# Kernel tuning notes

Measured on AMD Instinct MI355X. Metric: run time of the kernel, lower is better.

## Reference

```python
import jax, jax.numpy as jnp
import numpy as np

N_NODES = 50000
F_IN = 96
HIDDEN = 128
OUT = 64
N_EDGES = 800000


def setup_inputs() -> dict:
    key = jax.random.key(0)
    ks = jax.random.split(key, 8)
    x = jax.random.normal(ks[0], (N_NODES, F_IN), dtype=jnp.float32)
    edge_index = jax.random.randint(ks[1], (2, N_EDGES), 0, N_NODES, dtype=jnp.int64)
    s = 1.0 / np.sqrt(F_IN)
    W1_rel = jax.random.uniform(ks[2], (HIDDEN, F_IN), minval=-s, maxval=s, dtype=jnp.float32)
    b1 = jax.random.uniform(ks[3], (HIDDEN,), minval=-s, maxval=s, dtype=jnp.float32)
    W1_root = jax.random.uniform(ks[4], (HIDDEN, F_IN), minval=-s, maxval=s, dtype=jnp.float32)
    s2 = 1.0 / np.sqrt(HIDDEN)
    W2_rel = jax.random.uniform(ks[5], (OUT, HIDDEN), minval=-s2, maxval=s2, dtype=jnp.float32)
    b2 = jax.random.uniform(ks[6], (OUT,), minval=-s2, maxval=s2, dtype=jnp.float32)
    W2_root = jax.random.uniform(ks[7], (OUT, HIDDEN), minval=-s2, maxval=s2, dtype=jnp.float32)
    return {"x": x, "edge_index": edge_index, "W1_rel": W1_rel, "b1": b1,
            "W1_root": W1_root, "W2_rel": W2_rel, "b2": b2, "W2_root": W2_root}


def _graph_conv(x, src, dst, mask, W_rel, b, W_root):
    # messages = x[src] (masked to remove self-loops), sum-aggregated at dst
    msgs = x[src] * mask  # [E, F]
    agg = jax.ops.segment_sum(msgs, dst, num_segments=x.shape[0])  # [N, F]
    return agg @ W_rel.T + b + x @ W_root.T


def reference(x, edge_index, W1_rel, b1, W1_root, W2_rel, b2, W2_root):
    src, dst = edge_index[0], edge_index[1]
    # remove_self_loops: zero out contributions of edges with src == dst
    mask = (src != dst).astype(x.dtype)[:, None]  # [E, 1]
    h = jax.nn.relu(_graph_conv(x, src, dst, mask, W1_rel, b1, W1_root))
    out = _graph_conv(h, src, dst, mask, W2_rel, b2, W2_root)
    return out
```

## Files before the change

kernel.cpp:

```cpp
#include <hip/hip_runtime.h>


#define N_NODES 50000
#define F_IN    96
#define HIDDEN  128
#define OUT_F   64
#define DCAP    64

typedef __attribute__((ext_vector_type(8))) short short8;
typedef __attribute__((ext_vector_type(4))) float floatx4;

__device__ inline unsigned short f2bf(float f) {
    union { float f; unsigned u; } v; v.f = f;
    unsigned r = v.u + 0x7FFF + ((v.u >> 16) & 1);
    return (unsigned short)(r >> 16);
}
__device__ inline float bf2f(unsigned short b) {
    union { unsigned u; float f; } v; v.u = ((unsigned)b) << 16;
    return v.f;
}

__global__ __launch_bounds__(256) void setup_kernel(
    const float* __restrict__ x,
    const float* __restrict__ W1_rel, const float* __restrict__ W1_root,
    const float* __restrict__ W2_rel, const float* __restrict__ W2_root,
    unsigned short* __restrict__ xb, unsigned short* __restrict__ W1b,
    unsigned short* __restrict__ W2rb, unsigned short* __restrict__ W2sb,
    int* __restrict__ degz, int total8, int nzero)
{
    int i = blockIdx.x * 256 + threadIdx.x;
    if (i < total8) {
        const float4* p = (const float4*)(x + (size_t)i * 8);
        float4 v0 = p[0], v1 = p[1];
        short8 o;
        o[0] = (short)f2bf(v0.x); o[1] = (short)f2bf(v0.y);
        o[2] = (short)f2bf(v0.z); o[3] = (short)f2bf(v0.w);
        o[4] = (short)f2bf(v1.x); o[5] = (short)f2bf(v1.y);
        o[6] = (short)f2bf(v1.z); o[7] = (short)f2bf(v1.w);
        *(short8*)(xb + (size_t)i * 8) = o;
    }
    if (i < nzero) degz[i] = 0;
    if (i < 128 * 192) {
        int j = i / 192, k = i % 192;
        float v = (k < 96) ? W1_rel[j * 96 + k] : W1_root[j * 96 + k - 96];
        W1b[i] = f2bf(v);
    } else if (i < 128 * 192 + 64 * 128) {
        int i2 = i - 128 * 192;
        W2rb[i2] = f2bf(W2_rel[i2]);
    } else if (i < 128 * 192 + 2 * 64 * 128) {
        int i3 = i - 128 * 192 - 64 * 128;
        W2sb[i3] = f2bf(W2_root[i3]);
    }
}

__global__ __launch_bounds__(256) void place_kernel(
    const int* __restrict__ ei, int* __restrict__ deg,
    int* __restrict__ csr, int E, int slice_size)
{
    int sl = blockIdx.x & 7;
    int i4 = (blockIdx.x >> 3) * 256 + threadIdx.x;
    int E4 = E >> 2;
    if (i4 < E4) {
        int4 d4 = ((const int4*)(ei + E))[i4];
        int e0 = i4 * 4;
        int dd[4] = {d4.x, d4.y, d4.z, d4.w};
        #pragma unroll
        for (int k = 0; k < 4; ++k) {
            int d = dd[k];
            if ((unsigned)d >= (unsigned)N_NODES) continue;
            if (d / slice_size != sl) continue;
            int s = ei[e0 + k];
            if (s == d) continue;
            int r = atomicAdd(&deg[d], 1);
            if (r < DCAP) csr[d * DCAP + r] = s;
        }
    } else if (i4 == E4) {
        for (int e = E4 * 4; e < E; ++e) {
            int d = ei[E + e];
            if ((unsigned)d >= (unsigned)N_NODES) continue;
            if (d / slice_size != sl) continue;
            int s = ei[e];
            if (s == d) continue;
            int r = atomicAdd(&deg[d], 1);
            if (r < DCAP) csr[d * DCAP + r] = s;
        }
    }
}

template<int F>
__device__ inline void gather_row8(const unsigned short* __restrict__ feat,
                                   const int* __restrict__ csr, int j, int end,
                                   float* acc)
{
    const unsigned short* fc = feat;
    for (; j + 3 < end; j += 4) {
        int s0 = csr[j], s1 = csr[j + 1], s2 = csr[j + 2], s3 = csr[j + 3];
        s0 = ((unsigned)s0 < (unsigned)N_NODES) ? s0 : 0;
        s1 = ((unsigned)s1 < (unsigned)N_NODES) ? s1 : 0;
        s2 = ((unsigned)s2 < (unsigned)N_NODES) ? s2 : 0;
        s3 = ((unsigned)s3 < (unsigned)N_NODES) ? s3 : 0;
        short8 v0 = *(const short8*)(fc + (size_t)s0 * F);
        short8 v1 = *(const short8*)(fc + (size_t)s1 * F);
        short8 v2 = *(const short8*)(fc + (size_t)s2 * F);
        short8 v3 = *(const short8*)(fc + (size_t)s3 * F);
        #pragma unroll
        for (int i = 0; i < 8; ++i)
            acc[i] += (bf2f((unsigned short)v0[i]) + bf2f((unsigned short)v1[i]))
                    + (bf2f((unsigned short)v2[i]) + bf2f((unsigned short)v3[i]));
    }
    for (; j < end; ++j) {
        int s0 = csr[j];
        s0 = ((unsigned)s0 < (unsigned)N_NODES) ? s0 : 0;
        short8 v0 = *(const short8*)(fc + (size_t)s0 * F);
        #pragma unroll
        for (int i = 0; i < 8; ++i) acc[i] += bf2f((unsigned short)v0[i]);
    }
}

__global__ __launch_bounds__(256) void gemm1_fused(
    const unsigned short* __restrict__ xb, const unsigned short* __restrict__ W1b,
    const float* __restrict__ b1, const int* __restrict__ deg,
    const int* __restrict__ csr, unsigned short* __restrict__ h, int N)
{
    __shared__ __align__(16) unsigned short aggs[32][104];
    const int tid = threadIdx.x;
    const int node0 = blockIdx.x * 32;

    for (int task = tid; task < 384; task += 256) {
        int nl = task / 12, c = task % 12;
        int node = node0 + nl;
        float acc[8] = {};
        if (node < N) {
            int dg = deg[node];
            if (dg > DCAP) dg = DCAP;
            int j = node * DCAP;
            gather_row8<F_IN>(xb + c * 8, csr, j, j + dg, acc);
        }
        short8 o;
        #pragma unroll
        for (int i = 0; i < 8; ++i) o[i] = (short)f2bf(acc[i]);
        *(short8*)&aggs[nl][c * 8] = o;
    }
    __syncthreads();

    const int lane = tid & 63;
    const int wave = tid >> 6;
    const int m = lane & 15, quad = lane >> 4;
    const int node_base = node0 + (wave & 1) * 16;
    const int jt0 = (wave >> 1) * 4;
    int na = node_base + m;
    if (na >= N) na = N - 1;
    short8 a[6];
    #pragma unroll
    for (int c = 0; c < 3; ++c)
        a[c] = *(const short8*)&aggs[(wave & 1) * 16 + m][c * 32 + quad * 8];
    #pragma unroll
    for (int c = 0; c < 3; ++c)
        a[3 + c] = *(const short8*)(xb + (size_t)na * 96 + c * 32 + quad * 8);
    #pragma unroll
    for (int jt = 0; jt < 4; ++jt) {
        floatx4 acc = {0.f, 0.f, 0.f, 0.f};
        const unsigned short* wb = W1b + (size_t)((jt0 + jt) * 16 + m) * 192 + quad * 8;
        #pragma unroll
        for (int c = 0; c < 6; ++c) {
            short8 b = *(const short8*)(wb + c * 32);
            acc = __builtin_amdgcn_mfma_f32_16x16x32_bf16(a[c], b, acc, 0, 0, 0);
        }
        int col = (jt0 + jt) * 16 + m;
        float bv = b1[col];
        #pragma unroll
        for (int r = 0; r < 4; ++r) {
            int node = node_base + quad * 4 + r;
            if (node < N)
                h[(size_t)node * 128 + col] = f2bf(fmaxf(acc[r] + bv, 0.f));
        }
    }
}

__global__ __launch_bounds__(256) void gemm2_kernel(
    const unsigned short* __restrict__ h, const unsigned short* __restrict__ W2rb,
    unsigned short* __restrict__ t, int N)
{
    const int lane = threadIdx.x & 63;
    const int wave = threadIdx.x >> 6;
    const int node_base = blockIdx.x * 64 + wave * 16;
    const int m = lane & 15, quad = lane >> 4;
    int na = node_base + m;
    if (na >= N) na = N - 1;
    short8 a[4];
    #pragma unroll
    for (int c = 0; c < 4; ++c)
        a[c] = *(const short8*)(h + (size_t)na * 128 + c * 32 + quad * 8);
    #pragma unroll
    for (int jt = 0; jt < 4; ++jt) {
        floatx4 acc = {0.f, 0.f, 0.f, 0.f};
        const unsigned short* wb = W2rb + (size_t)(jt * 16 + m) * 128 + quad * 8;
        #pragma unroll
        for (int c = 0; c < 4; ++c) {
            short8 b = *(const short8*)(wb + c * 32);
            acc = __builtin_amdgcn_mfma_f32_16x16x32_bf16(a[c], b, acc, 0, 0, 0);
        }
        int col = jt * 16 + m;
        #pragma unroll
        for (int r = 0; r < 4; ++r) {
            int node = node_base + quad * 4 + r;
            if (node < N)
                t[(size_t)node * 64 + col] = f2bf(acc[r]);
        }
    }
}

__global__ __launch_bounds__(256) void gemm3_fused(
    const unsigned short* __restrict__ h, const unsigned short* __restrict__ tfeat,
    const unsigned short* __restrict__ W2sb, const float* __restrict__ b2,
    const int* __restrict__ deg, const int* __restrict__ csr,
    float* __restrict__ out, int N)
{
    __shared__ __align__(16) unsigned short agg2s[32][72];
    const int tid = threadIdx.x;
    const int node0 = blockIdx.x * 32;

    {
        int nl = tid / 8, c = tid % 8;
        int node = node0 + nl;
        float acc[8] = {};
        if (node < N) {
            int dg = deg[node];
            if (dg > DCAP) dg = DCAP;
            int j = node * DCAP;
            gather_row8<OUT_F>(tfeat + c * 8, csr, j, j + dg, acc);
        }
        short8 o;
        #pragma unroll
        for (int i = 0; i < 8; ++i) o[i] = (short)f2bf(acc[i]);
        *(short8*)&agg2s[nl][c * 8] = o;
    }
    __syncthreads();

    const int lane = tid & 63;
    const int wave = tid >> 6;
    const int m = lane & 15, quad = lane >> 4;
    const int node_base = node0 + (wave & 1) * 16;
    const int jt0 = (wave >> 1) * 2;
    int na = node_base + m;
    if (na >= N) na = N - 1;
    short8 a[4];
    #pragma unroll
    for (int c = 0; c < 4; ++c)
        a[c] = *(const short8*)(h + (size_t)na * 128 + c * 32 + quad * 8);
    #pragma unroll
    for (int jt = 0; jt < 2; ++jt) {
        floatx4 acc = {0.f, 0.f, 0.f, 0.f};
        const unsigned short* wb = W2sb + (size_t)((jt0 + jt) * 16 + m) * 128 + quad * 8;
        #pragma unroll
        for (int c = 0; c < 4; ++c) {
            short8 b = *(const short8*)(wb + c * 32);
            acc = __builtin_amdgcn_mfma_f32_16x16x32_bf16(a[c], b, acc, 0, 0, 0);
        }
        int col = (jt0 + jt) * 16 + m;
        float bv = b2[col];
        #pragma unroll
        for (int r = 0; r < 4; ++r) {
            int node = node_base + quad * 4 + r;
            if (node < N) {
                int nl = (wave & 1) * 16 + quad * 4 + r;
                float v = acc[r] + bv + bf2f(agg2s[nl][col]);
                out[(size_t)node * 64 + col] = v;
            }
        }
    }
}

extern "C" void kernel_launch(void* const* d_in, const int* in_sizes, int n_in,
                              void* d_out, int out_size, void* d_ws, size_t ws_size,
                              hipStream_t stream) {
    const float* x       = (const float*)d_in[0];
    const int*   ei      = (const int*)d_in[1];
    const float* W1_rel  = (const float*)d_in[2];
    const float* b1      = (const float*)d_in[3];
    const float* W1_root = (const float*)d_in[4];
    const float* W2_rel  = (const float*)d_in[5];
    const float* b2      = (const float*)d_in[6];
    const float* W2_root = (const float*)d_in[7];
    float* out = (float*)d_out;

    const int N = in_sizes[0] / F_IN;
    const int E = in_sizes[1] / 2;
    const int slice_size = ((N + 2047) / 2048) * 256;

    char* ws = (char*)d_ws;
    size_t p = 0;
    unsigned short* xb   = (unsigned short*)(ws + p); p += (size_t)N_NODES * F_IN * 2;
    unsigned short* h    = (unsigned short*)(ws + p); p += (size_t)N_NODES * HIDDEN * 2;
    unsigned short* t    = (unsigned short*)(ws + p); p += (size_t)N_NODES * OUT_F * 2;
    unsigned short* W1b  = (unsigned short*)(ws + p); p += (size_t)128 * 192 * 2;
    unsigned short* W2rb = (unsigned short*)(ws + p); p += (size_t)64 * 128 * 2;
    unsigned short* W2sb = (unsigned short*)(ws + p); p += (size_t)64 * 128 * 2;
    int* deg = (int*)(ws + p);  p += (size_t)N_NODES * 4;
    int* csr = (int*)(ws + p);  p += (size_t)N_NODES * DCAP * 4;

    {
        int total8 = N * F_IN / 8;
        setup_kernel<<<(total8 + 255) / 256, 256, 0, stream>>>(
            x, W1_rel, W1_root, W2_rel, W2_root, xb, W1b, W2rb, W2sb,
            deg, total8, N);
    }
    {
        int E4 = E >> 2;
        int bps = (E4 + 1 + 255) / 256;
        place_kernel<<<bps * 8, 256, 0, stream>>>(ei, deg, csr, E, slice_size);
    }

    const int tiles32 = (N + 31) / 32;

    gemm1_fused<<<tiles32, 256, 0, stream>>>(xb, W1b, b1, deg, csr, h, N);
    gemm2_kernel<<<(N + 63) / 64, 256, 0, stream>>>(h, W2rb, t, N);
    gemm3_fused<<<tiles32, 256, 0, stream>>>(h, t, W2sb, b2, deg, csr, out, N);
}
```

Before: 204.9 us.

## Split features into 32-column slices and gather each slice in separate passes

Node features and intermediates are stored as separate 32-column bf16 arrays (64-byte rows), and neighbor aggregation moves into a standalone gather kernel. That kernel processes one slice per pass so each pass's working set is smaller and more cache-resident. The GEMMs become separate kernels that read the pre-aggregated slices from global memory. This trades the fused gather+GEMM for extra kernel launches and extra global writes and reads of the aggregated features.

```diff
diff --git a/kernel.cpp b/kernel.cpp
--- a/kernel.cpp
+++ b/kernel.cpp
@@ -24,20 +24,23 @@
     const float* __restrict__ x,
     const float* __restrict__ W1_rel, const float* __restrict__ W1_root,
     const float* __restrict__ W2_rel, const float* __restrict__ W2_root,
-    unsigned short* __restrict__ xb, unsigned short* __restrict__ W1b,
+    unsigned short* __restrict__ xs0, unsigned short* __restrict__ xs1,
+    unsigned short* __restrict__ xs2, unsigned short* __restrict__ W1b,
     unsigned short* __restrict__ W2rb, unsigned short* __restrict__ W2sb,
     int* __restrict__ degz, int total8, int nzero)
 {
     int i = blockIdx.x * 256 + threadIdx.x;
     if (i < total8) {
-        const float4* p = (const float4*)(x + (size_t)i * 8);
+        int node = i / 12, q = i % 12;
+        const float4* p = (const float4*)(x + (size_t)node * 96 + q * 8);
         float4 v0 = p[0], v1 = p[1];
         short8 o;
         o[0] = (short)f2bf(v0.x); o[1] = (short)f2bf(v0.y);
         o[2] = (short)f2bf(v0.z); o[3] = (short)f2bf(v0.w);
         o[4] = (short)f2bf(v1.x); o[5] = (short)f2bf(v1.y);
         o[6] = (short)f2bf(v1.z); o[7] = (short)f2bf(v1.w);
-        *(short8*)(xb + (size_t)i * 8) = o;
+        unsigned short* arr = (q < 4) ? xs0 : (q < 8) ? xs1 : xs2;
+        *(short8*)(arr + (size_t)node * 32 + (q & 3) * 8) = o;
     }
     if (i < nzero) degz[i] = 0;
     if (i < 128 * 192) {
@@ -87,22 +90,36 @@
     }
 }
 
-template<int F>
-__device__ inline void gather_row8(const unsigned short* __restrict__ feat,
-                                   const int* __restrict__ csr, int j, int end,
-                                   float* acc)
-{
-    const unsigned short* fc = feat;
+__global__ __launch_bounds__(256) void gather_ksliced(
+    const unsigned short* __restrict__ f0, const unsigned short* __restrict__ f1,
+    const unsigned short* __restrict__ f2,
+    unsigned short* __restrict__ a0, unsigned short* __restrict__ a1,
+    unsigned short* __restrict__ a2,
+    const int* __restrict__ deg, const int* __restrict__ csr,
+    int N, int tilesPP)
+{
+    const int pass = blockIdx.x / tilesPP;
+    const unsigned short* __restrict__ F = (pass == 0) ? f0 : (pass == 1) ? f1 : f2;
+    unsigned short* __restrict__ A = (pass == 0) ? a0 : (pass == 1) ? a1 : a2;
+    const int tid = threadIdx.x;
+    const int node = (blockIdx.x % tilesPP) * 64 + (tid >> 2);
+    const int cq = tid & 3;
+    if (node >= N) return;
+    int dg = deg[node];
+    if (dg > DCAP) dg = DCAP;
+    int j = node * DCAP, end = j + dg;
+    float acc[8] = {};
+    const unsigned short* fc = F + cq * 8;
     for (; j + 3 < end; j += 4) {
         int s0 = csr[j], s1 = csr[j + 1], s2 = csr[j + 2], s3 = csr[j + 3];
         s0 = ((unsigned)s0 < (unsigned)N_NODES) ? s0 : 0;
         s1 = ((unsigned)s1 < (unsigned)N_NODES) ? s1 : 0;
         s2 = ((unsigned)s2 < (unsigned)N_NODES) ? s2 : 0;
         s3 = ((unsigned)s3 < (unsigned)N_NODES) ? s3 : 0;
-        short8 v0 = *(const short8*)(fc + (size_t)s0 * F);
-        short8 v1 = *(const short8*)(fc + (size_t)s1 * F);
-        short8 v2 = *(const short8*)(fc + (size_t)s2 * F);
-        short8 v3 = *(const short8*)(fc + (size_t)s3 * F);
+        short8 v0 = *(const short8*)(fc + (size_t)s0 * 32);
+        short8 v1 = *(const short8*)(fc + (size_t)s1 * 32);
+        short8 v2 = *(const short8*)(fc + (size_t)s2 * 32);
+        short8 v3 = *(const short8*)(fc + (size_t)s3 * 32);
         #pragma unroll
         for (int i = 0; i < 8; ++i)
             acc[i] += (bf2f((unsigned short)v0[i]) + bf2f((unsigned short)v1[i]))
@@ -111,62 +128,48 @@
     for (; j < end; ++j) {
         int s0 = csr[j];
         s0 = ((unsigned)s0 < (unsigned)N_NODES) ? s0 : 0;
-        short8 v0 = *(const short8*)(fc + (size_t)s0 * F);
+        short8 v0 = *(const short8*)(fc + (size_t)s0 * 32);
         #pragma unroll
         for (int i = 0; i < 8; ++i) acc[i] += bf2f((unsigned short)v0[i]);
     }
-}
-
-__global__ __launch_bounds__(256) void gemm1_fused(
-    const unsigned short* __restrict__ xb, const unsigned short* __restrict__ W1b,
-    const float* __restrict__ b1, const int* __restrict__ deg,
-    const int* __restrict__ csr, unsigned short* __restrict__ h, int N)
-{
-    __shared__ __align__(16) unsigned short aggs[32][104];
-    const int tid = threadIdx.x;
-    const int node0 = blockIdx.x * 32;
-
-    for (int task = tid; task < 384; task += 256) {
-        int nl = task / 12, c = task % 12;
-        int node = node0 + nl;
-        float acc[8] = {};
-        if (node < N) {
-            int dg = deg[node];
-            if (dg > DCAP) dg = DCAP;
-            int j = node * DCAP;
-            gather_row8<F_IN>(xb + c * 8, csr, j, j + dg, acc);
-        }
-        short8 o;
-        #pragma unroll
-        for (int i = 0; i < 8; ++i) o[i] = (short)f2bf(acc[i]);
-        *(short8*)&aggs[nl][c * 8] = o;
-    }
-    __syncthreads();
-
-    const int lane = tid & 63;
-    const int wave = tid >> 6;
+    short8 o;
+    #pragma unroll
+    for (int i = 0; i < 8; ++i) o[i] = (short)f2bf(acc[i]);
+    *(short8*)(A + (size_t)node * 32 + cq * 8) = o;
+}
+
+__global__ __launch_bounds__(256) void gemm1_kernel(
+    const unsigned short* __restrict__ a0, const unsigned short* __restrict__ a1,
+    const unsigned short* __restrict__ a2,
+    const unsigned short* __restrict__ xs0, const unsigned short* __restrict__ xs1,
+    const unsigned short* __restrict__ xs2,
+    const unsigned short* __restrict__ W1b, const float* __restrict__ b1,
+    unsigned short* __restrict__ h, int N)
+{
+    const int lane = threadIdx.x & 63;
+    const int wave = threadIdx.x >> 6;
+    const int node_base = blockIdx.x * 64 + wave * 16;
     const int m = lane & 15, quad = lane >> 4;
-    const int node_base = node0 + (wave & 1) * 16;
-    const int jt0 = (wave >> 1) * 4;
     int na = node_base + m;
     if (na >= N) na = N - 1;
+    const size_t ro = (size_t)na * 32 + quad * 8;
     short8 a[6];
-    #pragma unroll
-    for (int c = 0; c < 3; ++c)
-        a[c] = *(const short8*)&aggs[(wave & 1) * 16 + m][c * 32 + quad * 8];
-    #pragma unroll
-    for (int c = 0; c < 3; ++c)
-        a[3 + c] = *(const short8*)(xb + (size_t)na * 96 + c * 32 + quad * 8);
-    #pragma unroll
-    for (int jt = 0; jt < 4; ++jt) {
+    a[0] = *(const short8*)(a0 + ro);
+    a[1] = *(const short8*)(a1 + ro);
+    a[2] = *(const short8*)(a2 + ro);
+    a[3] = *(const short8*)(xs0 + ro);
+    a[4] = *(const short8*)(xs1 + ro);
+    a[5] = *(const short8*)(xs2 + ro);
+    #pragma unroll
+    for (int jt = 0; jt < 8; ++jt) {
         floatx4 acc = {0.f, 0.f, 0.f, 0.f};
-        const unsigned short* wb = W1b + (size_t)((jt0 + jt) * 16 + m) * 192 + quad * 8;
+        const unsigned short* wb = W1b + (size_t)(jt * 16 + m) * 192 + quad * 8;
         #pragma unroll
         for (int c = 0; c < 6; ++c) {
             short8 b = *(const short8*)(wb + c * 32);
             acc = __builtin_amdgcn_mfma_f32_16x16x32_bf16(a[c], b, acc, 0, 0, 0);
         }
-        int col = (jt0 + jt) * 16 + m;
+        int col = jt * 16 + m;
         float bv = b1[col];
         #pragma unroll
         for (int r = 0; r < 4; ++r) {
@@ -179,7 +182,7 @@
 
 __global__ __launch_bounds__(256) void gemm2_kernel(
     const unsigned short* __restrict__ h, const unsigned short* __restrict__ W2rb,
-    unsigned short* __restrict__ t, int N)
+    unsigned short* __restrict__ t0, unsigned short* __restrict__ t1, int N)
 {
     const int lane = threadIdx.x & 63;
     const int wave = threadIdx.x >> 6;
@@ -201,47 +204,27 @@
             acc = __builtin_amdgcn_mfma_f32_16x16x32_bf16(a[c], b, acc, 0, 0, 0);
         }
         int col = jt * 16 + m;
+        unsigned short* tarr = (col < 32) ? t0 : t1;
+        int co = col & 31;
         #pragma unroll
         for (int r = 0; r < 4; ++r) {
             int node = node_base + quad * 4 + r;
             if (node < N)
-                t[(size_t)node * 64 + col] = f2bf(acc[r]);
-        }
-    }
-}
-
-__global__ __launch_bounds__(256) void gemm3_fused(
-    const unsigned short* __restrict__ h, const unsigned short* __restrict__ tfeat,
-    const unsigned short* __restrict__ W2sb, const float* __restrict__ b2,
-    const int* __restrict__ deg, const int* __restrict__ csr,
+                tarr[(size_t)node * 32 + co] = f2bf(acc[r]);
+        }
+    }
+}
+
+__global__ __launch_bounds__(256) void gemm3_kernel(
+    const unsigned short* __restrict__ h, const unsigned short* __restrict__ W2sb,
+    const float* __restrict__ b2,
+    const unsigned short* __restrict__ g0, const unsigned short* __restrict__ g1,
     float* __restrict__ out, int N)
 {
-    __shared__ __align__(16) unsigned short agg2s[32][72];
-    const int tid = threadIdx.x;
-    const int node0 = blockIdx.x * 32;
-
-    {
-        int nl = tid / 8, c = tid % 8;
-        int node = node0 + nl;
-        float acc[8] = {};
-        if (node < N) {
-            int dg = deg[node];
-            if (dg > DCAP) dg = DCAP;
-            int j = node * DCAP;
-            gather_row8<OUT_F>(tfeat + c * 8, csr, j, j + dg, acc);
-        }
-        short8 o;
-        #pragma unroll
-        for (int i = 0; i < 8; ++i) o[i] = (short)f2bf(acc[i]);
-        *(short8*)&agg2s[nl][c * 8] = o;
-    }
-    __syncthreads();
-
-    const int lane = tid & 63;
-    const int wave = tid >> 6;
+    const int lane = threadIdx.x & 63;
+    const int wave = threadIdx.x >> 6;
+    const int node_base = blockIdx.x * 64 + wave * 16;
     const int m = lane & 15, quad = lane >> 4;
-    const int node_base = node0 + (wave & 1) * 16;
-    const int jt0 = (wave >> 1) * 2;
     int na = node_base + m;
     if (na >= N) na = N - 1;
     short8 a[4];
@@ -249,22 +232,23 @@
     for (int c = 0; c < 4; ++c)
         a[c] = *(const short8*)(h + (size_t)na * 128 + c * 32 + quad * 8);
     #pragma unroll
-    for (int jt = 0; jt < 2; ++jt) {
+    for (int jt = 0; jt < 4; ++jt) {
         floatx4 acc = {0.f, 0.f, 0.f, 0.f};
-        const unsigned short* wb = W2sb + (size_t)((jt0 + jt) * 16 + m) * 128 + quad * 8;
+        const unsigned short* wb = W2sb + (size_t)(jt * 16 + m) * 128 + quad * 8;
         #pragma unroll
         for (int c = 0; c < 4; ++c) {
             short8 b = *(const short8*)(wb + c * 32);
             acc = __builtin_amdgcn_mfma_f32_16x16x32_bf16(a[c], b, acc, 0, 0, 0);
         }
-        int col = (jt0 + jt) * 16 + m;
+        int col = jt * 16 + m;
         float bv = b2[col];
+        const unsigned short* garr = (col < 32) ? g0 : g1;
+        int co = col & 31;
         #pragma unroll
         for (int r = 0; r < 4; ++r) {
             int node = node_base + quad * 4 + r;
             if (node < N) {
-                int nl = (wave & 1) * 16 + quad * 4 + r;
-                float v = acc[r] + bv + bf2f(agg2s[nl][col]);
+                float v = acc[r] + bv + bf2f(garr[(size_t)node * 32 + co]);
                 out[(size_t)node * 64 + col] = v;
             }
         }
@@ -288,11 +272,21 @@
     const int E = in_sizes[1] / 2;
     const int slice_size = ((N + 2047) / 2048) * 256;
 
+    const size_t SLICE = (size_t)N_NODES * 32 * 2;
+
     char* ws = (char*)d_ws;
     size_t p = 0;
-    unsigned short* xb   = (unsigned short*)(ws + p); p += (size_t)N_NODES * F_IN * 2;
+    unsigned short* xs0  = (unsigned short*)(ws + p); p += SLICE;
+    unsigned short* xs1  = (unsigned short*)(ws + p); p += SLICE;
+    unsigned short* xs2  = (unsigned short*)(ws + p); p += SLICE;
+    unsigned short* ag0  = (unsigned short*)(ws + p); p += SLICE;
+    unsigned short* ag1  = (unsigned short*)(ws + p); p += SLICE;
+    unsigned short* ag2  = (unsigned short*)(ws + p); p += SLICE;
+    unsigned short* t0   = (unsigned short*)(ws + p); p += SLICE;
+    unsigned short* t1   = (unsigned short*)(ws + p); p += SLICE;
+    unsigned short* g0   = (unsigned short*)(ws + p); p += SLICE;
+    unsigned short* g1   = (unsigned short*)(ws + p); p += SLICE;
     unsigned short* h    = (unsigned short*)(ws + p); p += (size_t)N_NODES * HIDDEN * 2;
-    unsigned short* t    = (unsigned short*)(ws + p); p += (size_t)N_NODES * OUT_F * 2;
     unsigned short* W1b  = (unsigned short*)(ws + p); p += (size_t)128 * 192 * 2;
     unsigned short* W2rb = (unsigned short*)(ws + p); p += (size_t)64 * 128 * 2;
     unsigned short* W2sb = (unsigned short*)(ws + p); p += (size_t)64 * 128 * 2;
@@ -300,10 +294,10 @@
     int* csr = (int*)(ws + p);  p += (size_t)N_NODES * DCAP * 4;
 
     {
-        int total8 = N * F_IN / 8;
+        int total8 = N * 12;
         setup_kernel<<<(total8 + 255) / 256, 256, 0, stream>>>(
-            x, W1_rel, W1_root, W2_rel, W2_root, xb, W1b, W2rb, W2sb,
-            deg, total8, N);
+            x, W1_rel, W1_root, W2_rel, W2_root,
+            xs0, xs1, xs2, W1b, W2rb, W2sb, deg, total8, N);
     }
     {
         int E4 = E >> 2;
@@ -311,9 +305,15 @@
         place_kernel<<<bps * 8, 256, 0, stream>>>(ei, deg, csr, E, slice_size);
     }
 
-    const int tiles32 = (N + 31) / 32;
-
-    gemm1_fused<<<tiles32, 256, 0, stream>>>(xb, W1b, b1, deg, csr, h, N);
-    gemm2_kernel<<<(N + 63) / 64, 256, 0, stream>>>(h, W2rb, t, N);
-    gemm3_fused<<<tiles32, 256, 0, stream>>>(h, t, W2sb, b2, deg, csr, out, N);
-}
+    const int tiles64 = (N + 63) / 64;
+
+    gather_ksliced<<<tiles64 * 3, 256, 0, stream>>>(
+        xs0, xs1, xs2, ag0, ag1, ag2, deg, csr, N, tiles64);
+    gemm1_kernel<<<tiles64, 256, 0, stream>>>(
+        ag0, ag1, ag2, xs0, xs1, xs2, W1b, b1, h, N);
+
+    gemm2_kernel<<<tiles64, 256, 0, stream>>>(h, W2rb, t0, t1, N);
+    gather_ksliced<<<tiles64 * 2, 256, 0, stream>>>(
+        t0, t1, nullptr, g0, g1, nullptr, deg, csr, N, tiles64);
+    gemm3_kernel<<<tiles64, 256, 0, stream>>>(h, W2sb, b2, g0, g1, out, N);
+}
```

After: 237.2 us. 15.8% more time.

## Fuse setup with edge placement and fold layer-2 rel GEMM into layer-1 kernel

Applied to the files above, without the earlier changes.

Merges the bf16 conversion kernel and the CSR placement kernel into one launch, with block ranges split by role, and moves the degree zeroing to a memset. Layer-1 output tiles are also staged in shared memory so the W2_rel projection (t = h·W2_relᵀ) is computed in the same kernel, removing the separate gemm2 launch and its reread of h from global memory. This cuts launch count and some memory traffic. The cost is extra shared memory and a block barrier in the fused kernel, which may lower occupancy.

```diff
diff --git a/kernel.cpp b/kernel.cpp
--- a/kernel.cpp
+++ b/kernel.cpp
@@ -20,45 +20,45 @@
     return v.f;
 }
 
-__global__ __launch_bounds__(256) void setup_kernel(
+__global__ __launch_bounds__(256) void setup_place_kernel(
     const float* __restrict__ x,
     const float* __restrict__ W1_rel, const float* __restrict__ W1_root,
     const float* __restrict__ W2_rel, const float* __restrict__ W2_root,
+    const int* __restrict__ ei,
     unsigned short* __restrict__ xb, unsigned short* __restrict__ W1b,
     unsigned short* __restrict__ W2rb, unsigned short* __restrict__ W2sb,
-    int* __restrict__ degz, int total8, int nzero)
+    int* __restrict__ deg, int* __restrict__ csr,
+    int SB, int total8, int E, int slice_size)
 {
-    int i = blockIdx.x * 256 + threadIdx.x;
-    if (i < total8) {
-        const float4* p = (const float4*)(x + (size_t)i * 8);
-        float4 v0 = p[0], v1 = p[1];
-        short8 o;
-        o[0] = (short)f2bf(v0.x); o[1] = (short)f2bf(v0.y);
-        o[2] = (short)f2bf(v0.z); o[3] = (short)f2bf(v0.w);
-        o[4] = (short)f2bf(v1.x); o[5] = (short)f2bf(v1.y);
-        o[6] = (short)f2bf(v1.z); o[7] = (short)f2bf(v1.w);
-        *(short8*)(xb + (size_t)i * 8) = o;
-    }
-    if (i < nzero) degz[i] = 0;
-    if (i < 128 * 192) {
-        int j = i / 192, k = i % 192;
-        float v = (k < 96) ? W1_rel[j * 96 + k] : W1_root[j * 96 + k - 96];
-        W1b[i] = f2bf(v);
-    } else if (i < 128 * 192 + 64 * 128) {
-        int i2 = i - 128 * 192;
-        W2rb[i2] = f2bf(W2_rel[i2]);
-    } else if (i < 128 * 192 + 2 * 64 * 128) {
-        int i3 = i - 128 * 192 - 64 * 128;
-        W2sb[i3] = f2bf(W2_root[i3]);
-    }
-}
-
-__global__ __launch_bounds__(256) void place_kernel(
-    const int* __restrict__ ei, int* __restrict__ deg,
-    int* __restrict__ csr, int E, int slice_size)
-{
-    int sl = blockIdx.x & 7;
-    int i4 = (blockIdx.x >> 3) * 256 + threadIdx.x;
+    const int tid = threadIdx.x;
+    if ((int)blockIdx.x < SB) {
+        int i = blockIdx.x * 256 + tid;
+        if (i < total8) {
+            const float4* p = (const float4*)(x + (size_t)i * 8);
+            float4 v0 = p[0], v1 = p[1];
+            short8 o;
+            o[0] = (short)f2bf(v0.x); o[1] = (short)f2bf(v0.y);
+            o[2] = (short)f2bf(v0.z); o[3] = (short)f2bf(v0.w);
+            o[4] = (short)f2bf(v1.x); o[5] = (short)f2bf(v1.y);
+            o[6] = (short)f2bf(v1.z); o[7] = (short)f2bf(v1.w);
+            *(short8*)(xb + (size_t)i * 8) = o;
+        }
+        if (i < 128 * 192) {
+            int j = i / 192, k = i % 192;
+            float v = (k < 96) ? W1_rel[j * 96 + k] : W1_root[j * 96 + k - 96];
+            W1b[i] = f2bf(v);
+        } else if (i < 128 * 192 + 64 * 128) {
+            int i2 = i - 128 * 192;
+            W2rb[i2] = f2bf(W2_rel[i2]);
+        } else if (i < 128 * 192 + 2 * 64 * 128) {
+            int i3 = i - 128 * 192 - 64 * 128;
+            W2sb[i3] = f2bf(W2_root[i3]);
+        }
+        return;
+    }
+    int pb = blockIdx.x - SB;
+    int sl = pb & 7;
+    int i4 = (pb >> 3) * 256 + tid;
     int E4 = E >> 2;
     if (i4 < E4) {
         int4 d4 = ((const int4*)(ei + E))[i4];
@@ -117,12 +117,14 @@
     }
 }
 
-__global__ __launch_bounds__(256) void gemm1_fused(
+__global__ __launch_bounds__(256) void mega1_kernel(
     const unsigned short* __restrict__ xb, const unsigned short* __restrict__ W1b,
-    const float* __restrict__ b1, const int* __restrict__ deg,
-    const int* __restrict__ csr, unsigned short* __restrict__ h, int N)
+    const unsigned short* __restrict__ W2rb, const float* __restrict__ b1,
+    const int* __restrict__ deg, const int* __restrict__ csr,
+    unsigned short* __restrict__ h, unsigned short* __restrict__ t, int N)
 {
     __shared__ __align__(16) unsigned short aggs[32][104];
+    __shared__ __align__(16) unsigned short hs[32][136];
     const int tid = threadIdx.x;
     const int node0 = blockIdx.x * 32;
 
@@ -146,14 +148,15 @@
     const int lane = tid & 63;
     const int wave = tid >> 6;
     const int m = lane & 15, quad = lane >> 4;
-    const int node_base = node0 + (wave & 1) * 16;
+    const int nh = wave & 1;
+    const int node_base = node0 + nh * 16;
     const int jt0 = (wave >> 1) * 4;
     int na = node_base + m;
     if (na >= N) na = N - 1;
     short8 a[6];
     #pragma unroll
     for (int c = 0; c < 3; ++c)
-        a[c] = *(const short8*)&aggs[(wave & 1) * 16 + m][c * 32 + quad * 8];
+        a[c] = *(const short8*)&aggs[nh * 16 + m][c * 32 + quad * 8];
     #pragma unroll
     for (int c = 0; c < 3; ++c)
         a[3 + c] = *(const short8*)(xb + (size_t)na * 96 + c * 32 + quad * 8);
@@ -171,36 +174,29 @@
         #pragma unroll
         for (int r = 0; r < 4; ++r) {
             int node = node_base + quad * 4 + r;
-            if (node < N)
-                h[(size_t)node * 128 + col] = f2bf(fmaxf(acc[r] + bv, 0.f));
-        }
-    }
-}
-
-__global__ __launch_bounds__(256) void gemm2_kernel(
-    const unsigned short* __restrict__ h, const unsigned short* __restrict__ W2rb,
-    unsigned short* __restrict__ t, int N)
-{
-    const int lane = threadIdx.x & 63;
-    const int wave = threadIdx.x >> 6;
-    const int node_base = blockIdx.x * 64 + wave * 16;
-    const int m = lane & 15, quad = lane >> 4;
-    int na = node_base + m;
-    if (na >= N) na = N - 1;
-    short8 a[4];
+            float v = fmaxf(acc[r] + bv, 0.f);
+            unsigned short vb = f2bf(v);
+            hs[nh * 16 + quad * 4 + r][col] = vb;
+            if (node < N) h[(size_t)node * 128 + col] = vb;
+        }
+    }
+    __syncthreads();
+
+    const int jtt0 = (wave >> 1) * 2;
+    short8 a2[4];
     #pragma unroll
     for (int c = 0; c < 4; ++c)
-        a[c] = *(const short8*)(h + (size_t)na * 128 + c * 32 + quad * 8);
-    #pragma unroll
-    for (int jt = 0; jt < 4; ++jt) {
+        a2[c] = *(const short8*)&hs[nh * 16 + m][c * 32 + quad * 8];
+    #pragma unroll
+    for (int jt = 0; jt < 2; ++jt) {
         floatx4 acc = {0.f, 0.f, 0.f, 0.f};
-        const unsigned short* wb = W2rb + (size_t)(jt * 16 + m) * 128 + quad * 8;
+        const unsigned short* wb = W2rb + (size_t)((jtt0 + jt) * 16 + m) * 128 + quad * 8;
         #pragma unroll
         for (int c = 0; c < 4; ++c) {
             short8 b = *(const short8*)(wb + c * 32);
-            acc = __builtin_amdgcn_mfma_f32_16x16x32_bf16(a[c], b, acc, 0, 0, 0);
-        }
-        int col = jt * 16 + m;
+            acc = __builtin_amdgcn_mfma_f32_16x16x32_bf16(a2[c], b, acc, 0, 0, 0);
+        }
+        int col = (jtt0 + jt) * 16 + m;
         #pragma unroll
         for (int r = 0; r < 4; ++r) {
             int node = node_base + quad * 4 + r;
@@ -299,21 +295,22 @@
     int* deg = (int*)(ws + p);  p += (size_t)N_NODES * 4;
     int* csr = (int*)(ws + p);  p += (size_t)N_NODES * DCAP * 4;
 
+    hipMemsetAsync(deg, 0, (size_t)N * 4, stream);
+
     {
         int total8 = N * F_IN / 8;
-        setup_kernel<<<(total8 + 255) / 256, 256, 0, stream>>>(
-            x, W1_rel, W1_root, W2_rel, W2_root, xb, W1b, W2rb, W2sb,
-            deg, total8, N);
-    }
-    {
+        int SB = (total8 + 255) / 256;
         int E4 = E >> 2;
         int bps = (E4 + 1 + 255) / 256;
-        place_kernel<<<bps * 8, 256, 0, stream>>>(ei, deg, csr, E, slice_size);
+        int PB = bps * 8;
+        setup_place_kernel<<<SB + PB, 256, 0, stream>>>(
+            x, W1_rel, W1_root, W2_rel, W2_root, ei,
+            xb, W1b, W2rb, W2sb, deg, csr, SB, total8, E, slice_size);
     }
 
     const int tiles32 = (N + 31) / 32;
 
-    gemm1_fused<<<tiles32, 256, 0, stream>>>(xb, W1b, b1, deg, csr, h, N);
-    gemm2_kernel<<<(N + 63) / 64, 256, 0, stream>>>(h, W2rb, t, N);
+    mega1_kernel<<<tiles32, 256, 0, stream>>>(xb, W1b, W2rb, b1, deg, csr, h, t, N);
+
     gemm3_fused<<<tiles32, 256, 0, stream>>>(h, t, W2sb, b2, deg, csr, out, N);
 }
```

Result: faster. 198.6 us (-3.1%).
